# Optimization experiments

Measured on AMD Instinct MI355X. Metric: run time of the kernel, lower is better.

Reference implementation:

```python
import jax, jax.numpy as jnp
import numpy as np

NEG_INF = -1000000.0  # matches torch masked_fill constant


def setup_inputs() -> dict:
    key = jax.random.key(0)
    k1, k2, k3, k4 = jax.random.split(key, 4)
    B, Lq, Lk, d = 64, 1024, 1024, 64
    queries = jax.random.normal(k1, (B, Lq, d), dtype=jnp.float32)
    keys = jax.random.normal(k2, (B, Lk, d), dtype=jnp.float32)
    values = jax.random.normal(k3, (B, Lk, d), dtype=jnp.float32)
    valid_lens = jax.random.randint(k4, (B,), 0, 1024, dtype=jnp.int64)
    return {"queries": queries, "keys": keys, "values": values, "valid_lens": valid_lens}


def reference(queries, keys, values, valid_lens):
    d = queries.shape[-1]
    # [B, Lq, Lk] scores
    scores = jnp.einsum("bqd,bkd->bqk", queries, keys) / jnp.sqrt(jnp.float32(d))
    Lk = scores.shape[-1]
    # valid_lens is per-batch (dim 1 in torch): same mask across all query rows
    mask = jnp.arange(Lk)[None, None, :] < valid_lens[:, None, None]  # [B,1,Lk]
    scores = jnp.where(mask, scores, NEG_INF)
    attn = jax.nn.softmax(scores, axis=-1)
    # dropout p=0.0 -> identity
    return jnp.einsum("bqk,bkd->bqd", attn, values)
```

## Files before the change

### kernel.cpp

```cpp
#include <hip/hip_runtime.h>
#include <hip/hip_bf16.h>

#define NEG_BIG -1000000.0f

typedef __attribute__((ext_vector_type(8))) short short8;
typedef __attribute__((ext_vector_type(4))) short short4v;
typedef __attribute__((ext_vector_type(4))) float floatx4;

#if __has_builtin(__builtin_amdgcn_exp2f)
#define EXP2F(x) __builtin_amdgcn_exp2f(x)
#else
#define EXP2F(x) exp2f(x)
#endif

#if __has_builtin(__builtin_amdgcn_mfma_f32_16x16x16bf16_1k)
#define MFMA16(a, b, c) __builtin_amdgcn_mfma_f32_16x16x16bf16_1k(a, b, c, 0, 0, 0)
#else
static __device__ __forceinline__ floatx4 MFMA16_fn(short4v a, short4v b, floatx4 c) {
    floatx4 d;
    asm("v_mfma_f32_16x16x16_bf16 %0, %1, %2, %3\n\ts_nop 4"
        : "=v"(d) : "v"(a), "v"(b), "v"(c));
    return d;
}
#define MFMA16(a, b, c) MFMA16_fn(a, b, c)
#endif

#if __has_builtin(__builtin_amdgcn_permlane16_swap) && __has_builtin(__builtin_amdgcn_permlane32_swap)
static __device__ __forceinline__ float redmax16_32(float x) {
    auto a = __builtin_amdgcn_permlane16_swap(__float_as_int(x), __float_as_int(x), false, false);
    x = fmaxf(__int_as_float(a[0]), __int_as_float(a[1]));
    auto b = __builtin_amdgcn_permlane32_swap(__float_as_int(x), __float_as_int(x), false, false);
    return fmaxf(__int_as_float(b[0]), __int_as_float(b[1]));
}
static __device__ __forceinline__ float redsum16_32(float x) {
    auto a = __builtin_amdgcn_permlane16_swap(__float_as_int(x), __float_as_int(x), false, false);
    x = __int_as_float(a[0]) + __int_as_float(a[1]);
    auto b = __builtin_amdgcn_permlane32_swap(__float_as_int(x), __float_as_int(x), false, false);
    return __int_as_float(b[0]) + __int_as_float(b[1]);
}
#else
static __device__ __forceinline__ float redmax16_32(float x) {
    x = fmaxf(x, __shfl_xor(x, 16));
    return fmaxf(x, __shfl_xor(x, 32));
}
static __device__ __forceinline__ float redsum16_32(float x) {
    x += __shfl_xor(x, 16);
    return x + __shfl_xor(x, 32);
}
#endif

static __device__ __forceinline__ unsigned short bf16u(float f) {
    union { __hip_bfloat16 h; unsigned short u; } c;
    c.h = __float2bfloat16(f);
    return c.u;
}

static __device__ __forceinline__ short8 pack8(float4 a, float4 b) {
    union { short8 s; __hip_bfloat162 h[4]; } u;
    u.h[0] = __float22bfloat162_rn(make_float2(a.x, a.y));
    u.h[1] = __float22bfloat162_rn(make_float2(a.z, a.w));
    u.h[2] = __float22bfloat162_rn(make_float2(b.x, b.y));
    u.h[3] = __float22bfloat162_rn(make_float2(b.z, b.w));
    return u.s;
}

__global__ __launch_bounds__(256, 4)
void attn_fwd(const float* __restrict__ Q, const float* __restrict__ K,
              const float* __restrict__ V, const int* __restrict__ vlen,
              float* __restrict__ out)
{
    __shared__ __attribute__((aligned(16))) unsigned short K_lds[2][4096];
    __shared__ __attribute__((aligned(16))) unsigned short VT_lds[3][4096];

    const int bid  = blockIdx.x;
    const int orig = (bid & 7) * 128 + (bid >> 3);
    const int b    = orig >> 4;
    const int qc   = orig & 15;

    const int tid = threadIdx.x;
    const int l   = tid & 63;
    const int w   = tid >> 6;
    const int lr  = l & 15;
    const int lg  = l >> 4;

    const float* Qb = Q + (size_t)b * 65536;
    const float* Kb = K + (size_t)b * 65536;
    const float* Vb = V + (size_t)b * 65536;

    const int valid = vlen[b];
    const int kmax  = (valid == 0) ? 1024 : valid;
    const int ntile = (kmax + 63) >> 6;

    const float qscale = 0.18033688011112042f;
    short8 qf[2];
#pragma unroll
    for (int c = 0; c < 2; ++c) {
        const float* p = Qb + (size_t)(qc*64 + w*16 + lr) * 64 + c*32 + lg*8;
        float4 a = *(const float4*)p, bb = *(const float4*)(p + 4);
        a.x *= qscale; a.y *= qscale; a.z *= qscale; a.w *= qscale;
        bb.x *= qscale; bb.y *= qscale; bb.z *= qscale; bb.w *= qscale;
        qf[c] = pack8(a, bb);
    }

    floatx4 o[4];
#pragma unroll
    for (int n = 0; n < 4; ++n) o[n] = (floatx4){0.f, 0.f, 0.f, 0.f};
    float m = -INFINITY, lsum = 0.f;
    short4v pkp[4];

    const int row   = w * 16 + (l >> 2);
    const int cbase = (l & 3) * 16;

    float4 kra[4], vra[4];

#define LOAD_K(T) do {                                                      \
    const float* pk_ = Kb + (size_t)((T)*64 + row) * 64 + cbase;            \
    kra[0] = *(const float4*)pk_;       kra[1] = *(const float4*)(pk_ + 4); \
    kra[2] = *(const float4*)(pk_ + 8); kra[3] = *(const float4*)(pk_ + 12);\
    } while (0)

#define LOAD_V(T) do {                                                      \
    const float* pv_ = Vb + (size_t)((T)*64 + row) * 64 + cbase;            \
    vra[0] = *(const float4*)pv_;       vra[1] = *(const float4*)(pv_ + 4); \
    vra[2] = *(const float4*)(pv_ + 8); vra[3] = *(const float4*)(pv_ + 12);\
    } while (0)

#define WRITE_K(B) do {                                                     \
    const int _fk = (row & 7) * 8;                                          \
    *(short8*)&K_lds[B][row*64 + (cbase ^ _fk)]       = pack8(kra[0], kra[1]); \
    *(short8*)&K_lds[B][row*64 + ((cbase + 8) ^ _fk)] = pack8(kra[2], kra[3]); \
    } while (0)

#define WRITE_V(B) do {                                                     \
    _Pragma("unroll")                                                       \
    for (int j = 0; j < 16; ++j) {                                          \
        const int dv = cbase + j;                                           \
        const int fv = ((dv & 7) ^ (dv >> 3)) * 8;                          \
        VT_lds[B][dv*64 + (row ^ fv)] = bf16u(((const float*)&vra[j>>2])[j&3]); \
    } } while (0)

#define QK_MFMA(SA, KBUF) do {                                              \
    _Pragma("unroll")                                                       \
    for (int n = 0; n < 4; ++n) {                                           \
        const int kr_ = n*16 + lr;                                          \
        const int fk_ = (lr & 7) * 8;                                       \
        const short8 kf0 = *(const short8*)&K_lds[KBUF][kr_*64 + ((lg*8)      ^ fk_)]; \
        const short8 kf1 = *(const short8*)&K_lds[KBUF][kr_*64 + ((32 + lg*8) ^ fk_)]; \
        SA[n] = (floatx4){0.f, 0.f, 0.f, 0.f};                              \
        SA[n] = __builtin_amdgcn_mfma_f32_16x16x32_bf16(kf0, qf[0], SA[n], 0, 0, 0); \
        SA[n] = __builtin_amdgcn_mfma_f32_16x16x32_bf16(kf1, qf[1], SA[n], 0, 0, 0); \
    } } while (0)

#define PV_MFMA(VBUF) do {                                                  \
    _Pragma("unroll")                                                       \
    for (int kc = 0; kc < 4; ++kc) {                                        \
        _Pragma("unroll")                                                   \
        for (int n2 = 0; n2 < 4; ++n2) {                                    \
            const int dv_ = n2*16 + lr;                                     \
            const int fv_ = ((dv_ & 7) ^ (dv_ >> 3)) * 8;                   \
            const short4v vf = *(const short4v*)&VT_lds[VBUF][dv_*64 + ((kc*16 + lg*4) ^ fv_)]; \
            o[n2] = MFMA16(pkp[kc], vf, o[n2]);                             \
        }                                                                   \
    } } while (0)

#define SOFTMAX(SA, T) do {                                                 \
    const int _k0 = (T) * 64;                                               \
    if ((_k0 + 64) > valid) {                                               \
        const int kb_ = _k0 + lg*4;                                         \
        _Pragma("unroll")                                                   \
        for (int n = 0; n < 4; ++n)                                         \
        _Pragma("unroll")                                                   \
        for (int r = 0; r < 4; ++r)                                         \
            SA[n][r] = (kb_ + n*16 + r >= valid) ? NEG_BIG : SA[n][r];      \
    }                                                                       \
                                      \
    float m0_ = fmaxf(fmaxf(SA[0][0], SA[0][1]), SA[0][2]);                 \
    float m1_ = fmaxf(fmaxf(SA[0][3], SA[1][0]), SA[1][1]);                 \
    float m2_ = fmaxf(fmaxf(SA[1][2], SA[1][3]), SA[2][0]);                 \
    float m3_ = fmaxf(fmaxf(SA[2][1], SA[2][2]), SA[2][3]);                 \
    float m4_ = fmaxf(fmaxf(SA[3][0], SA[3][1]), SA[3][2]);                 \
    float rmax = fmaxf(fmaxf(fmaxf(m0_, m1_), fmaxf(m2_, m3_)),            \
                       fmaxf(m4_, SA[3][3]));                               \
    rmax = redmax16_32(rmax);                                               \
    if (!__all(rmax <= m + 11.0f)) {                                        \
        const float nm_ = fmaxf(m, rmax);                                   \
        const float sc_f = EXP2F(m - nm_);                                  \
        m = nm_;                                                            \
        lsum *= sc_f;                                                       \
        float sc_r[4];                                                      \
        _Pragma("unroll")                                                   \
        for (int r = 0; r < 4; ++r) sc_r[r] = __shfl(sc_f, lg*4 + r);       \
        _Pragma("unroll")                                                   \
        for (int n = 0; n < 4; ++n)                                         \
        _Pragma("unroll")                                                   \
        for (int r = 0; r < 4; ++r) o[n][r] *= sc_r[r];                     \
    }                                                                       \
    _Pragma("unroll")                                                       \
    for (int n = 0; n < 4; ++n)                                             \
    _Pragma("unroll")                                                       \
    for (int r = 0; r < 4; ++r) SA[n][r] = EXP2F(SA[n][r] - m);             \
                                            \
    float s0_ = (SA[0][0]+SA[0][1]) + (SA[0][2]+SA[0][3]);                  \
    float s1_ = (SA[1][0]+SA[1][1]) + (SA[1][2]+SA[1][3]);                  \
    float s2_ = (SA[2][0]+SA[2][1]) + (SA[2][2]+SA[2][3]);                  \
    float s3_ = (SA[3][0]+SA[3][1]) + (SA[3][2]+SA[3][3]);                  \
    lsum += redsum16_32((s0_ + s1_) + (s2_ + s3_));                         \
    _Pragma("unroll")                                                       \
    for (int n = 0; n < 4; ++n) {                                           \
        union { short4v s; __hip_bfloat162 h[2]; } u;                       \
        u.h[0] = __float22bfloat162_rn(make_float2(SA[n][0], SA[n][1]));    \
        u.h[1] = __float22bfloat162_rn(make_float2(SA[n][2], SA[n][3]));    \
        pkp[n] = u.s;                                                       \
    } } while (0)

    LOAD_K(0);
    LOAD_V(0);
    WRITE_K(0);
    WRITE_V(0);
    __syncthreads();

    {
        if (ntile > 1) { LOAD_K(1); LOAD_V(1); }
        floatx4 sc[4];
        __builtin_amdgcn_s_setprio(1);
        QK_MFMA(sc, 0);
        __builtin_amdgcn_s_setprio(0);
        if (ntile > 1) { WRITE_K(1); WRITE_V(1); }
        SOFTMAX(sc, 0);
        if (ntile > 1) __syncthreads();
    }

    int vr = 0, vw = 2;
    for (int t = 1; t < ntile; ++t) {
        const bool pf = (t + 1 < ntile);
        if (pf) { LOAD_K(t + 1); LOAD_V(t + 1); }

        floatx4 sc[4];
        __builtin_amdgcn_s_setprio(1);
        QK_MFMA(sc, t & 1);
        PV_MFMA(vr);
        __builtin_amdgcn_s_setprio(0);

        if (pf) { WRITE_K((t + 1) & 1); WRITE_V(vw); }
        SOFTMAX(sc, t);
        __syncthreads();

        vr = (vr == 2) ? 0 : vr + 1;
        vw = (vw == 2) ? 0 : vw + 1;
    }

    __builtin_amdgcn_s_setprio(1);
    PV_MFMA(vr);
    __builtin_amdgcn_s_setprio(0);

    const float inv = 1.0f / lsum;
    float inv_r[4];
#pragma unroll
    for (int r = 0; r < 4; ++r) inv_r[r] = __shfl(inv, lg*4 + r);

    float* Ob = out + (size_t)b * 65536;
#pragma unroll
    for (int n = 0; n < 4; ++n)
#pragma unroll
    for (int r = 0; r < 4; ++r) {
        const int q = qc*64 + w*16 + lg*4 + r;
        Ob[(size_t)q * 64 + n*16 + lr] = o[n][r] * inv_r[r];
    }
#undef LOAD_K
#undef LOAD_V
#undef WRITE_K
#undef WRITE_V
#undef QK_MFMA
#undef PV_MFMA
#undef SOFTMAX
}

extern "C" void kernel_launch(void* const* d_in, const int* in_sizes, int n_in,
                              void* d_out, int out_size, void* d_ws, size_t ws_size,
                              hipStream_t stream) {
    (void)in_sizes; (void)n_in; (void)d_ws; (void)ws_size; (void)out_size;
    const float* Q  = (const float*)d_in[0];
    const float* K  = (const float*)d_in[1];
    const float* V  = (const float*)d_in[2];
    const int*   vl = (const int*)d_in[3];
    float* O = (float*)d_out;
    attn_fwd<<<dim3(1024), dim3(256), 0, stream>>>(Q, K, V, vl, O);
}
```

Baseline: 44.54 us.

## Process two 16-row query sub-tiles per wave to reuse K/V tiles

Each block now handles 128 query rows instead of 64, with each wave owning two 16-row query sub-tiles. Every K and V fragment loaded from LDS feeds two MFMAs, and each block's global K/V loads and bf16 conversions are amortised over twice as many queries. The grid is halved to 512 blocks and launch bounds are lowered to 2 blocks per CU to allow the extra accumulator registers. The trade-off is fewer blocks (512 across the GPU) and lower occupancy, which leaves less latency hiding and worse load balance across the varying valid_lens.

```diff
diff --git a/kernel.cpp b/kernel.cpp
--- a/kernel.cpp
+++ b/kernel.cpp
@@ -64,7 +64,7 @@
     return u.s;
 }
 
-__global__ __launch_bounds__(256, 4)
+__global__ __launch_bounds__(256, 2)
 void attn_fwd(const float* __restrict__ Q, const float* __restrict__ K,
               const float* __restrict__ V, const int* __restrict__ vlen,
               float* __restrict__ out)
@@ -73,9 +73,9 @@
     __shared__ __attribute__((aligned(16))) unsigned short VT_lds[3][4096];
 
     const int bid  = blockIdx.x;
-    const int orig = (bid & 7) * 128 + (bid >> 3);
-    const int b    = orig >> 4;
-    const int qc   = orig & 15;
+    const int orig = (bid & 7) * 64 + (bid >> 3);
+    const int b    = orig >> 3;
+    const int qc   = orig & 7;
 
     const int tid = threadIdx.x;
     const int l   = tid & 63;
@@ -92,21 +92,27 @@
     const int ntile = (kmax + 63) >> 6;
 
     const float qscale = 0.18033688011112042f;
-    short8 qf[2];
+    short8 qf[2][2];
+#pragma unroll
+    for (int s = 0; s < 2; ++s)
 #pragma unroll
     for (int c = 0; c < 2; ++c) {
-        const float* p = Qb + (size_t)(qc*64 + w*16 + lr) * 64 + c*32 + lg*8;
+        const float* p = Qb + (size_t)(qc*128 + w*32 + s*16 + lr) * 64 + c*32 + lg*8;
         float4 a = *(const float4*)p, bb = *(const float4*)(p + 4);
         a.x *= qscale; a.y *= qscale; a.z *= qscale; a.w *= qscale;
         bb.x *= qscale; bb.y *= qscale; bb.z *= qscale; bb.w *= qscale;
-        qf[c] = pack8(a, bb);
-    }
-
-    floatx4 o[4];
-#pragma unroll
-    for (int n = 0; n < 4; ++n) o[n] = (floatx4){0.f, 0.f, 0.f, 0.f};
-    float m = -INFINITY, lsum = 0.f;
-    short4v pkp[4];
+        qf[s][c] = pack8(a, bb);
+    }
+
+    floatx4 o[2][4];
+    float m[2], lsum[2];
+    short4v pkp[2][4];
+#pragma unroll
+    for (int s = 0; s < 2; ++s) {
+#pragma unroll
+        for (int n = 0; n < 4; ++n) o[s][n] = (floatx4){0.f, 0.f, 0.f, 0.f};
+        m[s] = -INFINITY; lsum[s] = 0.f;
+    }
 
     const int row   = w * 16 + (l >> 2);
     const int cbase = (l & 3) * 16;
@@ -146,9 +152,12 @@
         const int fk_ = (lr & 7) * 8;                                       \
         const short8 kf0 = *(const short8*)&K_lds[KBUF][kr_*64 + ((lg*8)      ^ fk_)]; \
         const short8 kf1 = *(const short8*)&K_lds[KBUF][kr_*64 + ((32 + lg*8) ^ fk_)]; \
-        SA[n] = (floatx4){0.f, 0.f, 0.f, 0.f};                              \
-        SA[n] = __builtin_amdgcn_mfma_f32_16x16x32_bf16(kf0, qf[0], SA[n], 0, 0, 0); \
-        SA[n] = __builtin_amdgcn_mfma_f32_16x16x32_bf16(kf1, qf[1], SA[n], 0, 0, 0); \
+        _Pragma("unroll")                                                   \
+        for (int s = 0; s < 2; ++s) {                                       \
+            SA[s][n] = (floatx4){0.f, 0.f, 0.f, 0.f};                       \
+            SA[s][n] = __builtin_amdgcn_mfma_f32_16x16x32_bf16(kf0, qf[s][0], SA[s][n], 0, 0, 0); \
+            SA[s][n] = __builtin_amdgcn_mfma_f32_16x16x32_bf16(kf1, qf[s][1], SA[s][n], 0, 0, 0); \
+        }                                                                   \
     } } while (0)
 
 #define PV_MFMA(VBUF) do {                                                  \
@@ -159,7 +168,8 @@
             const int dv_ = n2*16 + lr;                                     \
             const int fv_ = ((dv_ & 7) ^ (dv_ >> 3)) * 8;                   \
             const short4v vf = *(const short4v*)&VT_lds[VBUF][dv_*64 + ((kc*16 + lg*4) ^ fv_)]; \
-            o[n2] = MFMA16(pkp[kc], vf, o[n2]);                             \
+            o[0][n2] = MFMA16(pkp[0][kc], vf, o[0][n2]);                    \
+            o[1][n2] = MFMA16(pkp[1][kc], vf, o[1][n2]);                    \
         }                                                                   \
     } } while (0)
 
@@ -168,49 +178,61 @@
     if ((_k0 + 64) > valid) {                                               \
         const int kb_ = _k0 + lg*4;                                         \
         _Pragma("unroll")                                                   \
+        for (int s = 0; s < 2; ++s)                                         \
+        _Pragma("unroll")                                                   \
         for (int n = 0; n < 4; ++n)                                         \
         _Pragma("unroll")                                                   \
         for (int r = 0; r < 4; ++r)                                         \
-            SA[n][r] = (kb_ + n*16 + r >= valid) ? NEG_BIG : SA[n][r];      \
+            SA[s][n][r] = (kb_ + n*16 + r >= valid) ? NEG_BIG : SA[s][n][r];\
     }                                                                       \
-                                      \
-    float m0_ = fmaxf(fmaxf(SA[0][0], SA[0][1]), SA[0][2]);                 \
-    float m1_ = fmaxf(fmaxf(SA[0][3], SA[1][0]), SA[1][1]);                 \
-    float m2_ = fmaxf(fmaxf(SA[1][2], SA[1][3]), SA[2][0]);                 \
-    float m3_ = fmaxf(fmaxf(SA[2][1], SA[2][2]), SA[2][3]);                 \
-    float m4_ = fmaxf(fmaxf(SA[3][0], SA[3][1]), SA[3][2]);                 \
-    float rmax = fmaxf(fmaxf(fmaxf(m0_, m1_), fmaxf(m2_, m3_)),            \
-                       fmaxf(m4_, SA[3][3]));                               \
-    rmax = redmax16_32(rmax);                                               \
-    if (!__all(rmax <= m + 11.0f)) {                                        \
-        const float nm_ = fmaxf(m, rmax);                                   \
-        const float sc_f = EXP2F(m - nm_);                                  \
-        m = nm_;                                                            \
-        lsum *= sc_f;                                                       \
-        float sc_r[4];                                                      \
-        _Pragma("unroll")                                                   \
-        for (int r = 0; r < 4; ++r) sc_r[r] = __shfl(sc_f, lg*4 + r);       \
-        _Pragma("unroll")                                                   \
-        for (int n = 0; n < 4; ++n)                                         \
-        _Pragma("unroll")                                                   \
-        for (int r = 0; r < 4; ++r) o[n][r] *= sc_r[r];                     \
+    float rmax[2];                                                          \
+    _Pragma("unroll")                                                       \
+    for (int s = 0; s < 2; ++s) {                                           \
+        float m0_ = fmaxf(fmaxf(SA[s][0][0], SA[s][0][1]), SA[s][0][2]);    \
+        float m1_ = fmaxf(fmaxf(SA[s][0][3], SA[s][1][0]), SA[s][1][1]);    \
+        float m2_ = fmaxf(fmaxf(SA[s][1][2], SA[s][1][3]), SA[s][2][0]);    \
+        float m3_ = fmaxf(fmaxf(SA[s][2][1], SA[s][2][2]), SA[s][2][3]);    \
+        float m4_ = fmaxf(fmaxf(SA[s][3][0], SA[s][3][1]), SA[s][3][2]);    \
+        rmax[s] = fmaxf(fmaxf(fmaxf(m0_, m1_), fmaxf(m2_, m3_)),           \
+                        fmaxf(m4_, SA[s][3][3]));                           \
+        rmax[s] = redmax16_32(rmax[s]);                                     \
     }                                                                       \
     _Pragma("unroll")                                                       \
+    for (int s = 0; s < 2; ++s) {                                           \
+        if (!__all(rmax[s] <= m[s] + 11.0f)) {                              \
+            const float nm_ = fmaxf(m[s], rmax[s]);                         \
+            const float sc_f = EXP2F(m[s] - nm_);                           \
+            m[s] = nm_;                                                     \
+            lsum[s] *= sc_f;                                                \
+            float sc_r[4];                                                  \
+            _Pragma("unroll")                                               \
+            for (int r = 0; r < 4; ++r) sc_r[r] = __shfl(sc_f, lg*4 + r);   \
+            _Pragma("unroll")                                               \
+            for (int n = 0; n < 4; ++n)                                     \
+            _Pragma("unroll")                                               \
+            for (int r = 0; r < 4; ++r) o[s][n][r] *= sc_r[r];              \
+        }                                                                   \
+    }                                                                       \
+    float rs[2] = {0.f, 0.f};                                               \
+    _Pragma("unroll")                                                       \
     for (int n = 0; n < 4; ++n)                                             \
     _Pragma("unroll")                                                       \
-    for (int r = 0; r < 4; ++r) SA[n][r] = EXP2F(SA[n][r] - m);             \
-                                            \
-    float s0_ = (SA[0][0]+SA[0][1]) + (SA[0][2]+SA[0][3]);                  \
-    float s1_ = (SA[1][0]+SA[1][1]) + (SA[1][2]+SA[1][3]);                  \
-    float s2_ = (SA[2][0]+SA[2][1]) + (SA[2][2]+SA[2][3]);                  \
-    float s3_ = (SA[3][0]+SA[3][1]) + (SA[3][2]+SA[3][3]);                  \
-    lsum += redsum16_32((s0_ + s1_) + (s2_ + s3_));                         \
+    for (int r = 0; r < 4; ++r) {                                           \
+        SA[0][n][r] = EXP2F(SA[0][n][r] - m[0]);                            \
+        SA[1][n][r] = EXP2F(SA[1][n][r] - m[1]);                            \
+        rs[0] += SA[0][n][r];                                               \
+        rs[1] += SA[1][n][r];                                               \
+    }                                                                       \
+    lsum[0] += redsum16_32(rs[0]);                                          \
+    lsum[1] += redsum16_32(rs[1]);                                          \
+    _Pragma("unroll")                                                       \
+    for (int s = 0; s < 2; ++s)                                             \
     _Pragma("unroll")                                                       \
     for (int n = 0; n < 4; ++n) {                                           \
-        union { short4v s; __hip_bfloat162 h[2]; } u;                       \
-        u.h[0] = __float22bfloat162_rn(make_float2(SA[n][0], SA[n][1]));    \
-        u.h[1] = __float22bfloat162_rn(make_float2(SA[n][2], SA[n][3]));    \
-        pkp[n] = u.s;                                                       \
+        union { short4v v; __hip_bfloat162 h[2]; } u;                       \
+        u.h[0] = __float22bfloat162_rn(make_float2(SA[s][n][0], SA[s][n][1])); \
+        u.h[1] = __float22bfloat162_rn(make_float2(SA[s][n][2], SA[s][n][3])); \
+        pkp[s][n] = u.v;                                                    \
     } } while (0)
 
     LOAD_K(0);
@@ -221,7 +243,7 @@
 
     {
         if (ntile > 1) { LOAD_K(1); LOAD_V(1); }
-        floatx4 sc[4];
+        floatx4 sc[2][4];
         __builtin_amdgcn_s_setprio(1);
         QK_MFMA(sc, 0);
         __builtin_amdgcn_s_setprio(0);
@@ -235,7 +257,7 @@
         const bool pf = (t + 1 < ntile);
         if (pf) { LOAD_K(t + 1); LOAD_V(t + 1); }
 
-        floatx4 sc[4];
+        floatx4 sc[2][4];
         __builtin_amdgcn_s_setprio(1);
         QK_MFMA(sc, t & 1);
         PV_MFMA(vr);
@@ -253,18 +275,20 @@
     PV_MFMA(vr);
     __builtin_amdgcn_s_setprio(0);
 
-    const float inv = 1.0f / lsum;
-    float inv_r[4];
-#pragma unroll
-    for (int r = 0; r < 4; ++r) inv_r[r] = __shfl(inv, lg*4 + r);
-
     float* Ob = out + (size_t)b * 65536;
 #pragma unroll
-    for (int n = 0; n < 4; ++n)
-#pragma unroll
-    for (int r = 0; r < 4; ++r) {
-        const int q = qc*64 + w*16 + lg*4 + r;
-        Ob[(size_t)q * 64 + n*16 + lr] = o[n][r] * inv_r[r];
+    for (int s = 0; s < 2; ++s) {
+        const float inv = 1.0f / lsum[s];
+        float inv_r[4];
+#pragma unroll
+        for (int r = 0; r < 4; ++r) inv_r[r] = __shfl(inv, lg*4 + r);
+#pragma unroll
+        for (int n = 0; n < 4; ++n)
+#pragma unroll
+        for (int r = 0; r < 4; ++r) {
+            const int q = qc*128 + w*32 + s*16 + lg*4 + r;
+            Ob[(size_t)q * 64 + n*16 + lr] = o[s][n][r] * inv_r[r];
+        }
     }
 #undef LOAD_K
 #undef LOAD_V
@@ -284,5 +308,5 @@
     const float* V  = (const float*)d_in[2];
     const int*   vl = (const int*)d_in[3];
     float* O = (float*)d_out;
-    attn_fwd<<<dim3(1024), dim3(256), 0, stream>>>(Q, K, V, vl, O);
-}
+    attn_fwd<<<dim3(512), dim3(256), 0, stream>>>(Q, K, V, vl, O);
+}
```

After: 39.48 us. 11.4% less time.
